# Kernel tuning notes

Hardware: AMD Instinct MI355X
Metric: run time of the kernel (lower is better)

The kernel has to match this reference:

```python
import jax, jax.numpy as jnp
import numpy as np

D_MODEL, N_HEADS, D_FF = 1024, 16, 4096
SCALE = 0.1          # lookup-activation input quantization step
NUM_BITS = 8
LEVELS = 1 << NUM_BITS   # 256
HALF = LEVELS // 2       # 128
MAX_EXP = 4
EPS = 1e-5


def pow2_weight(key, shape, max_exp=MAX_EXP):
    """Ternary power-of-two weights: values in {0, +/-2^{-e}}, e in [max_exp, max_exp+3].
    Exponent range keeps fan-in-1024 outputs O(1)."""
    k1, k2 = jax.random.split(key)
    sign = jax.random.randint(k1, shape, -1, 2).astype(jnp.float32)  # {-1,0,1}
    e = jax.random.randint(k2, shape, max_exp, max_exp + 4).astype(jnp.float32)
    return sign * jnp.exp2(-e)


def setup_inputs() -> dict:
    key = jax.random.key(0)
    ks = jax.random.split(key, 8)
    x = jax.random.normal(ks[0], (4, 2048, D_MODEL), dtype=jnp.float32)
    return {
        "x": x,
        "ln1_g": jnp.ones((D_MODEL,), jnp.float32),
        "ln1_b": jnp.zeros((D_MODEL,), jnp.float32),
        "wq": pow2_weight(ks[1], (D_MODEL, D_MODEL)),
        "wk": pow2_weight(ks[2], (D_MODEL, D_MODEL)),
        "wv": pow2_weight(ks[3], (D_MODEL, D_MODEL)),
        "wo": pow2_weight(ks[4], (D_MODEL, D_MODEL)),
        "ln2_g": jnp.ones((D_MODEL,), jnp.float32),
        "ln2_b": jnp.zeros((D_MODEL,), jnp.float32),
        "w1": pow2_weight(ks[5], (D_MODEL, D_FF)),
        "w2": pow2_weight(ks[6], (D_FF, D_MODEL)),
    }


def _layernorm(x, g, b):
    mu = jnp.mean(x, axis=-1, keepdims=True)
    var = jnp.var(x, axis=-1, keepdims=True)
    return (x - mu) * jax.lax.rsqrt(var + EPS) * g + b


def _lookup_act(x):
    # StructuredLookupActivation: quantize input to 2^num_bits levels, gather from
    # a precomputed GELU table (proved via Lasso lookup in the SNARK).
    grid = (jnp.arange(LEVELS, dtype=jnp.float32) - HALF) * SCALE
    table = jax.nn.gelu(grid)
    idx = jnp.clip(jnp.round(x / SCALE).astype(jnp.int32) + HALF, 0, LEVELS - 1)
    return table[idx]


def _linear_attention(x, wq, wk, wv, wo):
    B, S, D = x.shape
    H, Dh = N_HEADS, D // N_HEADS
    q = (x @ wq).reshape(B, S, H, Dh)
    k = (x @ wk).reshape(B, S, H, Dh)
    v = (x @ wv).reshape(B, S, H, Dh)
    # elu+1 feature map -> O(S*Dh^2) linear attention (no [S,S] scores)
    phi_q = jax.nn.elu(q) + 1.0
    phi_k = jax.nn.elu(k) + 1.0
    kv = jnp.einsum('bshd,bshe->bhde', phi_k, v)          # [B,H,Dh,Dh]
    z = jnp.sum(phi_k, axis=1)                            # [B,H,Dh]
    num = jnp.einsum('bshd,bhde->bshe', phi_q, kv)        # [B,S,H,Dh]
    den = jnp.einsum('bshd,bhd->bsh', phi_q, z)[..., None] + 1e-6
    out = (num / den).reshape(B, S, D)
    return out @ wo


def reference(x, ln1_g, ln1_b, wq, wk, wv, wo, ln2_g, ln2_b, w1, w2):
    # norm -> linear attention -> residual
    x = x + _linear_attention(_layernorm(x, ln1_g, ln1_b), wq, wk, wv, wo)
    # norm -> ternary FFN with lookup activation -> residual
    h = _layernorm(x, ln2_g, ln2_b)
    x = x + (_lookup_act(h @ w1) @ w2)
    return x
```

## Files before the change

### kernel.cpp

```cpp
#include <hip/hip_runtime.h>
#include <cstdint>
#include <cstddef>


#define D_MODEL 1024
#define SEQ     2048
#define BATCH   4
#define NTOK    8192
#define NHEADS  16
#define DH      64
#define DFF     4096
#define KVCH    16
#define CHROWS  (SEQ / KVCH)
#define PSTRIDE 4160

typedef _Float16 half8 __attribute__((ext_vector_type(8)));
typedef float f32x4 __attribute__((ext_vector_type(4)));

__device__ __forceinline__ unsigned short f2h(float x) {
  _Float16 h = (_Float16)x;
  union { _Float16 h; unsigned short u; } c; c.h = h; return c.u;
}
__device__ __forceinline__ float h2f(unsigned short u) {
  union { unsigned short u; _Float16 h; } c; c.u = u; return (float)c.h;
}

__device__ __forceinline__ float phi_act(float x) {
  return x > 0.f ? x + 1.f : expf(x);
}

__device__ __forceinline__ float gelu_exact(float v) {
  float c = 0.7978845608028654f;
  float t = tanhf(c * (v + 0.044715f * v * v * v));
  return 0.5f * v * (1.f + t);
}

__device__ __forceinline__ void gl_lds16(const void* g, void* l) {
  __builtin_amdgcn_global_load_lds(
      (const __attribute__((address_space(1))) unsigned int*)g,
      (__attribute__((address_space(3))) unsigned int*)l, 16, 0, 0);
}

__global__ __launch_bounds__(256) void convT(const float* __restrict__ W,
                                             unsigned short* __restrict__ WT,
                                             int K, int N) {
  __shared__ float tile[64][65];
  int kb = blockIdx.y << 6, nb = blockIdx.x << 6;
  int t = threadIdx.x;
  int rr = t >> 4, cc = (t & 15) << 2;
#pragma unroll
  for (int i = 0; i < 4; ++i) {
    int r = rr + (i << 4);
    float4 v = *(const float4*)(W + (size_t)(kb + r) * N + nb + cc);
    tile[r][cc] = v.x; tile[r][cc + 1] = v.y; tile[r][cc + 2] = v.z; tile[r][cc + 3] = v.w;
  }
  __syncthreads();
#pragma unroll
  for (int i = 0; i < 4; ++i) {
    int n = rr + (i << 4);
    ushort4 o;
    o.x = f2h(tile[cc + 0][n]); o.y = f2h(tile[cc + 1][n]);
    o.z = f2h(tile[cc + 2][n]); o.w = f2h(tile[cc + 3][n]);
    *(ushort4*)(WT + (size_t)(nb + n) * K + kb + cc) = o;
  }
}

__global__ __launch_bounds__(256) void ln_kernel(const float* __restrict__ X,
                                                 const float* __restrict__ g,
                                                 const float* __restrict__ b,
                                                 unsigned short* __restrict__ Y) {
  int tok = blockIdx.x;
  int t = threadIdx.x;
  const float4* xr = (const float4*)(X + (size_t)tok * D_MODEL);
  float4 v = xr[t];
  float s  = v.x + v.y + v.z + v.w;
  float s2 = v.x * v.x + v.y * v.y + v.z * v.z + v.w * v.w;
#pragma unroll
  for (int o = 32; o > 0; o >>= 1) {
    s  += __shfl_down(s, o);
    s2 += __shfl_down(s2, o);
  }
  __shared__ float red[8];
  __shared__ float mu_s, rs_s;
  int wid = t >> 6;
  if ((t & 63) == 0) { red[wid] = s; red[wid + 4] = s2; }
  __syncthreads();
  if (t == 0) {
    float ts  = red[0] + red[1] + red[2] + red[3];
    float ts2 = red[4] + red[5] + red[6] + red[7];
    float mu  = ts * (1.f / D_MODEL);
    float var = ts2 * (1.f / D_MODEL) - mu * mu;
    mu_s = mu;
    rs_s = rsqrtf(var + 1e-5f);
  }
  __syncthreads();
  float mu = mu_s, rs = rs_s;
  float4 gv = ((const float4*)g)[t];
  float4 bv = ((const float4*)b)[t];
  ushort4 hv;
  hv.x = f2h((v.x - mu) * rs * gv.x + bv.x);
  hv.y = f2h((v.y - mu) * rs * gv.y + bv.y);
  hv.z = f2h((v.z - mu) * rs * gv.z + bv.z);
  hv.w = f2h((v.w - mu) * rs * gv.w + bv.w);
  ((ushort4*)(Y + (size_t)tok * D_MODEL))[t] = hv;
}

template <int EP, int BK>
__global__ __launch_bounds__(256, (BK == 64) ? 4 : 2) void mfma_gemm(
    const unsigned short* __restrict__ A,
    const unsigned short* __restrict__ BT,
    void* Cv, const float* R, int N, int K) {
  constexpr int SEGS = BK / 8;
  constexpr int RPC  = 64 / SEGS;
  constexpr int NJ   = 32 / RPC;
  __shared__ unsigned short smem[2 * 128 * BK];
  __shared__ float gtab[EP == 3 ? 256 : 1];
  unsigned short* sA = smem;
  unsigned short* sB = smem + 128 * BK;

  int t = threadIdx.x;
  if (EP == 3) gtab[t & 255] = gelu_exact((float)((t & 255) - 128) * 0.1f);

  int bm, bn;
  {
    int L = blockIdx.y * gridDim.x + blockIdx.x;
    if ((gridDim.y & 7) == 0) {
      int xcd = L & 7, wi = L >> 3;
      int mPerX = gridDim.y >> 3;
      bm = xcd * mPerX + wi / gridDim.x;
      bn = wi % gridDim.x;
    } else {
      bn = blockIdx.x; bm = blockIdx.y;
    }
  }

  int w = t >> 6, l = t & 63;
  int lrow = l / SEGS;
  int lseg = l & (SEGS - 1);
  int m0 = bm << 7;
  int n0 = bn << 7;
  size_t strideB = (size_t)K * 2;

  const char* gA[NJ]; const char* gB[NJ];
  int ldsOff[NJ];
#pragma unroll
  for (int j = 0; j < NJ; ++j) {
    int row = (w << 5) + j * RPC + lrow;
    int gso = (lseg ^ (row & 7)) << 4;
    gA[j] = (const char*)A + (size_t)(m0 + row) * strideB + gso;
    gB[j] = (const char*)BT + (size_t)(n0 + row) * strideB + gso;
    ldsOff[j] = ((w << 5) + j * RPC) * BK;
  }

  int wm = w >> 1, wn = w & 1;
  int m16 = l & 15, qd = l >> 4;

  f32x4 acc[4][4];
#pragma unroll
  for (int i = 0; i < 4; ++i)
#pragma unroll
    for (int j = 0; j < 4; ++j) acc[i][j] = (f32x4){0.f, 0.f, 0.f, 0.f};

  for (int k0 = 0; k0 < K; k0 += BK) {
    size_t kb = (size_t)k0 * 2;
#pragma unroll
    for (int j = 0; j < NJ; ++j) {
      gl_lds16(gA[j] + kb, sA + ldsOff[j]);
      gl_lds16(gB[j] + kb, sB + ldsOff[j]);
    }
    __syncthreads();
#pragma unroll
    for (int kk = 0; kk < BK / 32; ++kk) {
      int ksb = (kk << 2) + qd;
      half8 af[4], bf[4];
#pragma unroll
      for (int mt = 0; mt < 4; ++mt) {
        int r = (wm << 6) + (mt << 4) + m16;
        int slot = ksb ^ (r & 7);
        af[mt] = *(const half8*)(sA + r * BK + (slot << 3));
      }
#pragma unroll
      for (int nt = 0; nt < 4; ++nt) {
        int r = (wn << 6) + (nt << 4) + m16;
        int slot = ksb ^ (r & 7);
        bf[nt] = *(const half8*)(sB + r * BK + (slot << 3));
      }
#pragma unroll
      for (int mt = 0; mt < 4; ++mt)
#pragma unroll
        for (int nt = 0; nt < 4; ++nt)
          acc[mt][nt] = __builtin_amdgcn_mfma_f32_16x16x32_f16(af[mt], bf[nt], acc[mt][nt], 0, 0, 0);
    }
    __syncthreads();
  }

  int sel = n0 >> 10;
  size_t slab = (size_t)sel * ((size_t)NTOK * D_MODEL);
  int colL = (n0 & 1023) + (wn << 6) + m16;

  int colBase = n0 + (wn << 6) + m16;
#pragma unroll
  for (int mt = 0; mt < 4; ++mt) {
    int rBase = m0 + (wm << 6) + (mt << 4) + (qd << 2);
#pragma unroll
    for (int nt = 0; nt < 4; ++nt) {
      int col = colBase + (nt << 4);
#pragma unroll
      for (int i = 0; i < 4; ++i) {
        float v = acc[mt][nt][i];
        if (EP == 4) {
          if (sel < 2) v = phi_act(v);
          size_t idx = slab + (size_t)(rBase + i) * D_MODEL + colL + (nt << 4);
          ((unsigned short*)Cv)[idx] = f2h(v);
        } else {
          size_t idx = (size_t)(rBase + i) * N + col;
          if (EP == 2)      ((float*)Cv)[idx] = R[idx] + v;
          else if (EP == 3) {
            float r = rintf(v / 0.1f);
            int iq = (int)r + 128;
            iq = iq < 0 ? 0 : (iq > 255 ? 255 : iq);
            ((unsigned short*)Cv)[idx] = f2h(gtab[iq]);
          } else          ((float*)Cv)[idx] = v;
        }
      }
    }
  }
}

__global__ __launch_bounds__(256) void kvz_partial(const unsigned short* __restrict__ PK,
                                                   const unsigned short* __restrict__ V,
                                                   float* __restrict__ P) {
  int c = blockIdx.x, bh = blockIdx.y;
  int b = bh >> 4, h = bh & 15;
  __shared__ float pk[8][64];
  __shared__ float vv[8][64];
  int t = threadIdx.x;
  const size_t base = ((size_t)b * SEQ + (size_t)c * CHROWS) * D_MODEL + h * DH;
  int u = t & 127;
  int lrow = u >> 4;
  int lcol = (u & 15) << 2;
  bool isV = (t >= 128);
  const unsigned short* src = isV ? V : PK;
  int dkb = (t >> 4) << 2;
  int deb = (t & 15) << 2;
  float acc[4][4] = {};
  float zacc = 0.f;
  for (int s0 = 0; s0 < CHROWS; s0 += 8) {
    ushort4 ld = *(const ushort4*)(src + base + (size_t)(s0 + lrow) * D_MODEL + lcol);
    float f0 = h2f(ld.x), f1 = h2f(ld.y), f2 = h2f(ld.z), f3 = h2f(ld.w);
    __syncthreads();
    if (isV) { vv[lrow][lcol] = f0; vv[lrow][lcol+1] = f1; vv[lrow][lcol+2] = f2; vv[lrow][lcol+3] = f3; }
    else     { pk[lrow][lcol] = f0; pk[lrow][lcol+1] = f1; pk[lrow][lcol+2] = f2; pk[lrow][lcol+3] = f3; }
    __syncthreads();
#pragma unroll
    for (int ss = 0; ss < 8; ++ss) {
      float4 a  = *(const float4*)&pk[ss][dkb];
      float4 bb = *(const float4*)&vv[ss][deb];
      acc[0][0] += a.x * bb.x; acc[0][1] += a.x * bb.y; acc[0][2] += a.x * bb.z; acc[0][3] += a.x * bb.w;
      acc[1][0] += a.y * bb.x; acc[1][1] += a.y * bb.y; acc[1][2] += a.y * bb.z; acc[1][3] += a.y * bb.w;
      acc[2][0] += a.z * bb.x; acc[2][1] += a.z * bb.y; acc[2][2] += a.z * bb.z; acc[2][3] += a.z * bb.w;
      acc[3][0] += a.w * bb.x; acc[3][1] += a.w * bb.y; acc[3][2] += a.w * bb.z; acc[3][3] += a.w * bb.w;
    }
    if (t < 64) {
#pragma unroll
      for (int ss = 0; ss < 8; ++ss) zacc += pk[ss][t];
    }
  }
  float* Pb = P + ((size_t)c * 64 + bh) * PSTRIDE;
#pragma unroll
  for (int i = 0; i < 4; ++i) {
    float4 o; o.x = acc[i][0]; o.y = acc[i][1]; o.z = acc[i][2]; o.w = acc[i][3];
    *(float4*)(Pb + (size_t)(dkb + i) * DH + deb) = o;
  }
  if (t < 64) Pb[4096 + t] = zacc;
}

__global__ __launch_bounds__(256) void kvz_reduce(const float* __restrict__ P,
                                                  float* __restrict__ KV,
                                                  float* __restrict__ Z) {
  int bh = blockIdx.x;
  int t = threadIdx.x;
  for (int i = t; i < PSTRIDE; i += 256) {
    float s = 0.f;
#pragma unroll
    for (int c = 0; c < KVCH; ++c)
      s += P[((size_t)c * 64 + bh) * PSTRIDE + i];
    if (i < 4096) KV[(size_t)bh * 4096 + i] = s;
    else          Z[(size_t)bh * 64 + (i - 4096)] = s;
  }
}

__global__ __launch_bounds__(256) void attn_kernel(const unsigned short* __restrict__ PQ,
                                                   const float* __restrict__ KVm,
                                                   const float* __restrict__ Z,
                                                   unsigned short* __restrict__ O) {
  int s0 = blockIdx.x << 6;
  int h = blockIdx.y, b = blockIdx.z;
  __shared__ float Pqt[64][64];
  __shared__ float Kv[64][64];
  __shared__ float den[64];
  __shared__ float zsh[64];
  int t = threadIdx.x;
  size_t qbase  = ((size_t)b * SEQ + s0) * D_MODEL + h * DH;
  size_t kvbase = (size_t)(b * NHEADS + h) * (DH * DH);
  int r0 = t >> 4;
  int c4 = (t & 15) << 2;
#pragma unroll
  for (int rr = 0; rr < 4; ++rr) {
    int row = r0 + (rr << 4);
    *(float4*)&Kv[row][c4] = *(const float4*)(KVm + kvbase + (size_t)row * DH + c4);
    ushort4 q = *(const ushort4*)(PQ + qbase + (size_t)row * D_MODEL + c4);
    Pqt[c4 + 0][row] = h2f(q.x);
    Pqt[c4 + 1][row] = h2f(q.y);
    Pqt[c4 + 2][row] = h2f(q.z);
    Pqt[c4 + 3][row] = h2f(q.w);
  }
  if (t < 16) *(float4*)&zsh[t << 2] = *(const float4*)(Z + (size_t)(b * NHEADS + h) * DH + (t << 2));
  __syncthreads();
  if (t < 64) {
    float d_ = 1e-6f;
#pragma unroll
    for (int dd = 0; dd < 64; ++dd) d_ += Pqt[dd][t] * zsh[dd];
    den[t] = d_;
  }
  __syncthreads();
  int tokb = (t >> 4) << 2, eb = (t & 15) << 2;
  float acc[4][4] = {};
#pragma unroll 8
  for (int dd = 0; dd < 64; ++dd) {
    float4 a  = *(const float4*)&Pqt[dd][tokb];
    float4 bb = *(const float4*)&Kv[dd][eb];
    acc[0][0] += a.x * bb.x; acc[0][1] += a.x * bb.y; acc[0][2] += a.x * bb.z; acc[0][3] += a.x * bb.w;
    acc[1][0] += a.y * bb.x; acc[1][1] += a.y * bb.y; acc[1][2] += a.y * bb.z; acc[1][3] += a.y * bb.w;
    acc[2][0] += a.z * bb.x; acc[2][1] += a.z * bb.y; acc[2][2] += a.z * bb.z; acc[2][3] += a.z * bb.w;
    acc[3][0] += a.w * bb.x; acc[3][1] += a.w * bb.y; acc[3][2] += a.w * bb.z; acc[3][3] += a.w * bb.w;
  }
#pragma unroll
  for (int i = 0; i < 4; ++i) {
    float dv = den[tokb + i];
    ushort4 hv;
    hv.x = f2h(acc[i][0] / dv);
    hv.y = f2h(acc[i][1] / dv);
    hv.z = f2h(acc[i][2] / dv);
    hv.w = f2h(acc[i][3] / dv);
    size_t oidx = ((size_t)b * SEQ + s0 + tokb + i) * D_MODEL + h * DH + eb;
    *(ushort4*)(O + oidx) = hv;
  }
}

extern "C" void kernel_launch(void* const* d_in, const int* in_sizes, int n_in,
                              void* d_out, int out_size, void* d_ws, size_t ws_size,
                              hipStream_t stream) {
  const float* x    = (const float*)d_in[0];
  const float* ln1g = (const float*)d_in[1];
  const float* ln1b = (const float*)d_in[2];
  const float* wq   = (const float*)d_in[3];
  const float* wk   = (const float*)d_in[4];
  const float* wv   = (const float*)d_in[5];
  const float* wo   = (const float*)d_in[6];
  const float* ln2g = (const float*)d_in[7];
  const float* ln2b = (const float*)d_in[8];
  const float* w1   = (const float*)d_in[9];
  const float* w2   = (const float*)d_in[10];
  float* out = (float*)d_out;
  char* ws = (char*)d_ws;

  const size_t MB = 1024 * 1024;
  unsigned short* xn   = (unsigned short*)(ws);
  unsigned short* qkv  = (unsigned short*)(ws + 32 * MB);
  unsigned short* phiq = qkv;
  unsigned short* phik = qkv + (size_t)NTOK * D_MODEL;
  unsigned short* vbuf = qkv + 2 * (size_t)NTOK * D_MODEL;
  unsigned short* ffn  = (unsigned short*)(ws + 32 * MB);
  unsigned short* w1T  = (unsigned short*)(ws + 96 * MB);
  unsigned short* w2T  = (unsigned short*)(ws + 104 * MB);
  unsigned short* woT  = (unsigned short*)(ws + 128 * MB);

  unsigned short* wqkvT = (unsigned short*)d_out;
  float* kvP = (float*)((char*)d_out + 6 * MB);
  float* kv  = (float*)((char*)d_out + 24 * MB);
  float* z   = (float*)((char*)d_out + 25 * MB);

  dim3 blk(256);
  dim3 gcD(D_MODEL / 64, D_MODEL / 64);

  convT<<<gcD, blk, 0, stream>>>(wq, wqkvT, D_MODEL, D_MODEL);
  convT<<<gcD, blk, 0, stream>>>(wk, wqkvT + (size_t)D_MODEL * D_MODEL, D_MODEL, D_MODEL);
  convT<<<gcD, blk, 0, stream>>>(wv, wqkvT + 2 * (size_t)D_MODEL * D_MODEL, D_MODEL, D_MODEL);
  convT<<<gcD, blk, 0, stream>>>(wo, woT, D_MODEL, D_MODEL);

  ln_kernel<<<NTOK, blk, 0, stream>>>(x, ln1g, ln1b, xn);

  dim3 gQKV(3 * D_MODEL / 128, NTOK / 128);
  mfma_gemm<4, 64><<<gQKV, blk, 0, stream>>>(xn, wqkvT, qkv, nullptr, 3 * D_MODEL, D_MODEL);

  kvz_partial<<<dim3(KVCH, BATCH * NHEADS), blk, 0, stream>>>(phik, vbuf, kvP);
  kvz_reduce<<<BATCH * NHEADS, blk, 0, stream>>>(kvP, kv, z);

  attn_kernel<<<dim3(SEQ / 64, NHEADS, BATCH), blk, 0, stream>>>(phiq, kv, z, xn);

  convT<<<dim3(DFF / 64, D_MODEL / 64), blk, 0, stream>>>(w1, w1T, D_MODEL, DFF);
  convT<<<dim3(D_MODEL / 64, DFF / 64), blk, 0, stream>>>(w2, w2T, DFF, D_MODEL);

  dim3 gD(D_MODEL / 128, NTOK / 128);
  mfma_gemm<2, 128><<<gD, blk, 0, stream>>>(xn, woT, out, x, D_MODEL, D_MODEL);

  ln_kernel<<<NTOK, blk, 0, stream>>>(out, ln2g, ln2b, xn);

  dim3 gF(DFF / 128, NTOK / 128);
  mfma_gemm<3, 64><<<gF, blk, 0, stream>>>(xn, w1T, ffn, nullptr, DFF, D_MODEL);

  mfma_gemm<2, 128><<<gD, blk, 0, stream>>>(ffn, w2T, out, out, D_MODEL, DFF);
}
```

Measured before the change: 454.1 us.

## Merge four weight transposes into one launch and change LDS swizzle pattern

Replaces the four separate convT launches for wq/wk/wv/wo with one batched convT4 kernel indexed by blockIdx.z, removing three launch overheads. It also changes the GEMM LDS XOR swizzle from row&7 to (row^(row>>3))&7, applied consistently on the global-load and LDS-read sides, to reduce LDS bank conflicts on fragment reads. The swizzle only changes which slot each row's segment lands in and keeps the data the same.

```diff
diff --git a/kernel.cpp b/kernel.cpp
--- a/kernel.cpp
+++ b/kernel.cpp
@@ -35,10 +35,44 @@
   return 0.5f * v * (1.f + t);
 }
 
+__device__ __forceinline__ int frow(int r) {
+  return (r ^ (r >> 3)) & 7;
+}
+
 __device__ __forceinline__ void gl_lds16(const void* g, void* l) {
   __builtin_amdgcn_global_load_lds(
       (const __attribute__((address_space(1))) unsigned int*)g,
       (__attribute__((address_space(3))) unsigned int*)l, 16, 0, 0);
+}
+
+__global__ __launch_bounds__(256) void convT4(const float* __restrict__ W0,
+                                              const float* __restrict__ W1,
+                                              const float* __restrict__ W2,
+                                              const float* __restrict__ W3,
+                                              unsigned short* __restrict__ D0,
+                                              unsigned short* __restrict__ D3) {
+  __shared__ float tile[64][65];
+  int zz = blockIdx.z;
+  const float* W = zz == 0 ? W0 : zz == 1 ? W1 : zz == 2 ? W2 : W3;
+  unsigned short* WT = zz < 3 ? (D0 + (size_t)zz * D_MODEL * D_MODEL) : D3;
+  int kb = blockIdx.y << 6, nb = blockIdx.x << 6;
+  int t = threadIdx.x;
+  int rr = t >> 4, cc = (t & 15) << 2;
+#pragma unroll
+  for (int i = 0; i < 4; ++i) {
+    int r = rr + (i << 4);
+    float4 v = *(const float4*)(W + (size_t)(kb + r) * D_MODEL + nb + cc);
+    tile[r][cc] = v.x; tile[r][cc + 1] = v.y; tile[r][cc + 2] = v.z; tile[r][cc + 3] = v.w;
+  }
+  __syncthreads();
+#pragma unroll
+  for (int i = 0; i < 4; ++i) {
+    int n = rr + (i << 4);
+    ushort4 o;
+    o.x = f2h(tile[cc + 0][n]); o.y = f2h(tile[cc + 1][n]);
+    o.z = f2h(tile[cc + 2][n]); o.w = f2h(tile[cc + 3][n]);
+    *(ushort4*)(WT + (size_t)(nb + n) * D_MODEL + kb + cc) = o;
+  }
 }
 
 __global__ __launch_bounds__(256) void convT(const float* __restrict__ W,
@@ -146,7 +180,7 @@
 #pragma unroll
   for (int j = 0; j < NJ; ++j) {
     int row = (w << 5) + j * RPC + lrow;
-    int gso = (lseg ^ (row & 7)) << 4;
+    int gso = (lseg ^ frow(row)) << 4;
     gA[j] = (const char*)A + (size_t)(m0 + row) * strideB + gso;
     gB[j] = (const char*)BT + (size_t)(n0 + row) * strideB + gso;
     ldsOff[j] = ((w << 5) + j * RPC) * BK;
@@ -176,13 +210,13 @@
 #pragma unroll
       for (int mt = 0; mt < 4; ++mt) {
         int r = (wm << 6) + (mt << 4) + m16;
-        int slot = ksb ^ (r & 7);
+        int slot = ksb ^ frow(r);
         af[mt] = *(const half8*)(sA + r * BK + (slot << 3));
       }
 #pragma unroll
       for (int nt = 0; nt < 4; ++nt) {
         int r = (wn << 6) + (nt << 4) + m16;
-        int slot = ksb ^ (r & 7);
+        int slot = ksb ^ frow(r);
         bf[nt] = *(const half8*)(sB + r * BK + (slot << 3));
       }
 #pragma unroll
@@ -382,12 +416,9 @@
   float* z   = (float*)((char*)d_out + 25 * MB);
 
   dim3 blk(256);
-  dim3 gcD(D_MODEL / 64, D_MODEL / 64);
-
-  convT<<<gcD, blk, 0, stream>>>(wq, wqkvT, D_MODEL, D_MODEL);
-  convT<<<gcD, blk, 0, stream>>>(wk, wqkvT + (size_t)D_MODEL * D_MODEL, D_MODEL, D_MODEL);
-  convT<<<gcD, blk, 0, stream>>>(wv, wqkvT + 2 * (size_t)D_MODEL * D_MODEL, D_MODEL, D_MODEL);
-  convT<<<gcD, blk, 0, stream>>>(wo, woT, D_MODEL, D_MODEL);
+
+  convT4<<<dim3(D_MODEL / 64, D_MODEL / 64, 4), blk, 0, stream>>>(
+      wq, wk, wv, wo, wqkvT, woT);
 
   ln_kernel<<<NTOK, blk, 0, stream>>>(x, ln1g, ln1b, xn);
 
```

Result: no change. 459.9 us (+1.3%).
